# Performance work log

Measured on AMD Instinct MI355X. Metric: run time of the kernel, lower is better.

Reference implementation:

```python
import jax, jax.numpy as jnp
import numpy as np


def _leaky(x):
    return jnp.where(x >= 0, x, 0.01 * x)  # nn.LeakyReLU default slope


def _conv1x1(x, w):
    # x: [B, C, H, W], w: [O, C] (1x1 conv == per-pixel channel GEMM)
    return jnp.einsum('bchw,oc->bohw', x, w)


def setup_inputs() -> dict:
    key = jax.random.key(0)
    ks = jax.random.split(key, 12)

    def kaiming(k, o, c):  # kaiming_normal_ fan_out, relu gain, 1x1 kernel
        return jax.random.normal(k, (o, c), jnp.float32) * np.float32(np.sqrt(2.0 / o))

    lr_feature = jax.random.normal(ks[0], (1, 32, 256, 512), jnp.float32)
    hr_feature = jax.random.normal(ks[1], (1, 32, 512, 1024), jnp.float32)
    return {
        'lr_feature': lr_feature,
        'hr_feature': hr_feature,
        's1_w0': kaiming(ks[2], 128, 128),
        's1_w1': kaiming(ks[3], 64, 128),
        's1_w2': kaiming(ks[4], 32, 64),
        's1_w3': kaiming(ks[5], 16, 32),
        's1_w4': kaiming(ks[6], 8, 16),
        's1_w5': kaiming(ks[7], 1, 8),
        's2_w0': kaiming(ks[8], 3, 3),
        's2_w1': kaiming(ks[9], 2, 3),
        's2_w2': kaiming(ks[10], 1, 2),
        'fuse_w': jnp.ones((1, 2), jnp.float32),  # fuse weight initialized to 1
    }


def reference(lr_feature, hr_feature, s1_w0, s1_w1, s1_w2, s1_w3, s1_w4, s1_w5,
              s2_w0, s2_w1, s2_w2, fuse_w):
    scale = hr_feature.shape[-1] // lr_feature.shape[-1]  # static python int (=2, even)
    Hh, Wh = hr_feature.shape[-2], hr_feature.shape[-1]

    # nearest-neighbor upsample of lr_feature by `scale` (expand/view trick in torch)
    lr_up = jnp.repeat(jnp.repeat(lr_feature, scale, axis=2), scale, axis=3)

    # representation: [B, 128, Hh, Wh]
    rep = jnp.concatenate(
        [lr_up, hr_feature, lr_up * hr_feature, (lr_up - hr_feature) ** 2], axis=1)

    # similarity_measure1: 1x1-conv MLP chain 128->128->64->32->16->8->1
    o = _leaky(_conv1x1(rep, s1_w0))
    o = _leaky(_conv1x1(o, s1_w1))
    o = _leaky(_conv1x1(o, s1_w2))
    o = _leaky(_conv1x1(o, s1_w3))
    o = _conv1x1(o, s1_w4)
    weights1 = _conv1x1(o, s1_w5)  # [B, 1, Hh, Wh]

    # distance matrix (even-scale branch): 3 channels [dx, dy, norm]
    v = jnp.arange(-(scale // 2), scale // 2 + 1, dtype=jnp.float32)
    m = v.shape[0] // 2
    v = jnp.concatenate([v[:m], v[m + 1:]])  # drop center -> length `scale`
    d0 = jnp.broadcast_to(v[None, :], (scale, scale))
    dm = jnp.stack([d0, d0.T, jnp.sqrt(d0 ** 2 + d0.T ** 2)], axis=0)  # [3,s,s]
    dm = jnp.tile(dm, (1, Hh // scale, Wh // scale))[None]  # [1, 3, Hh, Wh]

    # similarity_measure2: 3->3->2->1
    w2 = _leaky(_conv1x1(dm, s2_w0))
    w2 = _leaky(_conv1x1(w2, s2_w1))
    weights2 = _conv1x1(w2, s2_w2)  # [1, 1, Hh, Wh]

    # fuse (weight forced non-negative via abs, as in forward's .data mutation)
    mapping = _conv1x1(jnp.concatenate([weights1, weights2], axis=1), jnp.abs(fuse_w))
    return mapping
```

## Files before the change

### kernel.cpp

```cpp
#include <hip/hip_runtime.h>

typedef short v8s __attribute__((ext_vector_type(8)));
typedef float v4f __attribute__((ext_vector_type(4)));

#define Wh   1024
#define HWh  (1024 * 512)
#define Wlr  512
#define HWlr (512 * 256)

#define THREADS 768
#define WAVES   12
#define NBLK    256
#define SLOTS   64
#define MAXIT   6

#define HALF_STRIDE 2052
#define ACT_SHORTS  (2 * HALF_STRIDE)
#define WF_N         53
#define WFRAG_SHORTS (WF_N * 512)
#define LDS_BYTES   ((WFRAG_SHORTS + WAVES * ACT_SHORTS) * 2)

__device__ __forceinline__ unsigned short f2bf(float f) {
    union { float f; unsigned u; } v; v.f = f;
    unsigned r = v.u + 0x7FFFu + ((v.u >> 16) & 1u);
    return (unsigned short)(r >> 16);
}
__device__ __forceinline__ unsigned pk2(float a, float b) {
    union { float f; unsigned u; } ua, ub;
    ua.f = a; ub.f = b;
    return __builtin_amdgcn_perm(ub.u + 0x8000u, ua.u + 0x8000u, 0x07060302u);
}
__device__ __forceinline__ float leaky(float x) { return fmaxf(x, 0.01f * x); }

__device__ __forceinline__ void ep_write(unsigned short* buf, int h, int c0, int p, uint2 v) {
    *(uint2*)(buf + h * HALF_STRIDE + (c0 >> 5) * 512 +
              (((c0 >> 3) & 3) * 16 + p) * 8 + (c0 & 7)) = v;
}
__device__ __forceinline__ void stq(unsigned short* buf, int px, int pass, int cq,
                                    int c, unsigned lo, unsigned hi) {
    *(uint2*)(buf + (px >> 4) * HALF_STRIDE + c * 512 +
              (pass * 16 + (px & 15)) * 8 + 4 * cq) = (uint2){lo, hi};
}

__global__ __launch_bounds__(THREADS, 3)
void cmfsm_kernel(const float* __restrict__ lr, const float* __restrict__ hr,
                  const float* __restrict__ w0g, const float* __restrict__ w1g,
                  const float* __restrict__ w2g, const float* __restrict__ w3g,
                  const float* __restrict__ w4g, const float* __restrict__ w5g,
                  const float* __restrict__ t0g, const float* __restrict__ t1g,
                  const float* __restrict__ t2g, const float* __restrict__ fwg,
                  float* __restrict__ out)
{
    extern __shared__ unsigned short smem[];
    unsigned short* wfrag = smem;
    unsigned short* actS  = smem + WFRAG_SHORTS;

    const int tid  = threadIdx.x;
    const int lane = tid & 63;
    const int wv   = tid >> 6;
    const int p    = lane & 15;
    const int q    = lane >> 4;
    const int px   = lane & 31;
    const int cq   = lane >> 5;

    for (int e = tid; e < 32 * 64; e += THREADS) {
        int f = e >> 6, l = e & 63;
        int mt = f >> 2, ks = f & 3, pp = l & 15, qq = l >> 4;
        const float* src = w0g + (mt * 16 + pp) * 128 + ks * 32 + qq * 8;
        unsigned short* dst = wfrag + f * 512 + l * 8;
#pragma unroll
        for (int j = 0; j < 8; ++j) dst[j] = f2bf(src[j]);
    }
    for (int e = tid; e < 16 * 64; e += THREADS) {
        int f = e >> 6, l = e & 63;
        int mt = f >> 2, ks = f & 3, pp = l & 15, qq = l >> 4;
        const float* src = w1g + (mt * 16 + pp) * 128 + ks * 32 + qq * 8;
        unsigned short* dst = wfrag + (32 + f) * 512 + l * 8;
#pragma unroll
        for (int j = 0; j < 8; ++j) dst[j] = f2bf(src[j]);
    }
    if (tid < 4 * 64) {
        int f = tid >> 6, l = tid & 63;
        int mt = f >> 1, ks = f & 1, pp = l & 15, qq = l >> 4;
        const float* src = w2g + (mt * 16 + pp) * 64 + ks * 32 + qq * 8;
        unsigned short* dst = wfrag + (48 + f) * 512 + l * 8;
#pragma unroll
        for (int j = 0; j < 8; ++j) dst[j] = f2bf(src[j]);
    }
    if (tid < 64) {
        int l = tid, pp = l & 15, qq = l >> 4;
        const float* src = w3g + pp * 32 + qq * 8;
        unsigned short* dst = wfrag + 52 * 512 + l * 8;
#pragma unroll
        for (int j = 0; j < 8; ++j) dst[j] = f2bf(src[j]);
    }

    float w45[4];
#pragma unroll
    for (int r = 0; r < 4; ++r) {
        float s = 0.f;
#pragma unroll
        for (int j = 0; j < 8; ++j) s += w5g[j] * w4g[j * 16 + q * 4 + r];
        w45[r] = s;
    }

    float w2tab[4];
#pragma unroll
    for (int yp = 0; yp < 2; ++yp)
#pragma unroll
        for (int xp = 0; xp < 2; ++xp) {
            float i0 = xp ? 1.f : -1.f;
            float i1 = yp ? 1.f : -1.f;
            float i2 = 1.41421356237309505f;
            float h0[3], h1[2];
            for (int o = 0; o < 3; ++o)
                h0[o] = leaky(t0g[o*3+0]*i0 + t0g[o*3+1]*i1 + t0g[o*3+2]*i2);
            for (int o = 0; o < 2; ++o)
                h1[o] = leaky(t1g[o*3+0]*h0[0] + t1g[o*3+1]*h0[1] + t1g[o*3+2]*h0[2]);
            w2tab[yp*2+xp] = t2g[0]*h1[0] + t2g[1]*h1[1];
        }
    const float fa = fabsf(fwg[0]);
    const float fb = fabsf(fwg[1]);

    __syncthreads();

    unsigned short* B = actS + wv * ACT_SHORTS;
    const v4f z4 = (v4f){0.f, 0.f, 0.f, 0.f};

    for (int it = 0; it < MAXIT; ++it) {
        const int s = it * WAVES + wv;
        if (s >= SLOTS) break;
        const int gbase = (blockIdx.x * SLOTS + s) * 32;
        const int y     = gbase >> 10;
        const float* hr_it = hr + gbase;
        const float* lr_it = lr + (y >> 1) * Wlr + ((gbase & 1023) >> 1);

#pragma unroll
        for (int pass = 0; pass < 4; ++pass) {
            const int ch = pass * 8 + cq * 4;
            float h0 = hr_it[(size_t)(ch + 0) * HWh + px];
            float h1 = hr_it[(size_t)(ch + 1) * HWh + px];
            float h2 = hr_it[(size_t)(ch + 2) * HWh + px];
            float h3 = hr_it[(size_t)(ch + 3) * HWh + px];
            float l0 = lr_it[(size_t)(ch + 0) * HWlr + (px >> 1)];
            float l1 = lr_it[(size_t)(ch + 1) * HWlr + (px >> 1)];
            float l2 = lr_it[(size_t)(ch + 2) * HWlr + (px >> 1)];
            float l3 = lr_it[(size_t)(ch + 3) * HWlr + (px >> 1)];
            stq(B, px, pass, cq, 0, pk2(l0, l1), pk2(l2, l3));
            stq(B, px, pass, cq, 1, pk2(h0, h1), pk2(h2, h3));
            stq(B, px, pass, cq, 2, pk2(l0*h0, l1*h1), pk2(l2*h2, l3*h3));
            float d0 = l0-h0, d1 = l1-h1, d2 = l2-h2, d3 = l3-h3;
            stq(B, px, pass, cq, 3, pk2(d0*d0, d1*d1), pk2(d2*d2, d3*d3));
        }

        {
            v8s bfr[4][2];
#pragma unroll
            for (int ks = 0; ks < 4; ++ks) {
                bfr[ks][0] = *(const v8s*)(B + ks * 512 + lane * 8);
                bfr[ks][1] = *(const v8s*)(B + HALF_STRIDE + ks * 512 + lane * 8);
            }
#pragma unroll
            for (int mh = 0; mh < 2; ++mh) {
                v4f acc[4][2];
#pragma unroll
                for (int ks = 0; ks < 4; ++ks)
#pragma unroll
                    for (int mi = 0; mi < 4; ++mi) {
                        v8s a = *(const v8s*)(wfrag + ((mh*4+mi)*4 + ks) * 512 + lane * 8);
                        acc[mi][0] = __builtin_amdgcn_mfma_f32_16x16x32_bf16(
                            a, bfr[ks][0], ks == 0 ? z4 : acc[mi][0], 0, 0, 0);
                        acc[mi][1] = __builtin_amdgcn_mfma_f32_16x16x32_bf16(
                            a, bfr[ks][1], ks == 0 ? z4 : acc[mi][1], 0, 0, 0);
                    }
#pragma unroll
                for (int mi = 0; mi < 4; ++mi) {
                    const int c0 = 16 * (mh * 4 + mi) + 4 * q;
#pragma unroll
                    for (int h = 0; h < 2; ++h) {
                        uint2 v;
                        v.x = pk2(leaky(acc[mi][h][0]), leaky(acc[mi][h][1]));
                        v.y = pk2(leaky(acc[mi][h][2]), leaky(acc[mi][h][3]));
                        ep_write(B, h, c0, p, v);
                    }
                }
            }
        }

        {
            v8s bfr[4][2];
#pragma unroll
            for (int ks = 0; ks < 4; ++ks) {
                bfr[ks][0] = *(const v8s*)(B + ks * 512 + lane * 8);
                bfr[ks][1] = *(const v8s*)(B + HALF_STRIDE + ks * 512 + lane * 8);
            }
            v4f acc[4][2];
#pragma unroll
            for (int ks = 0; ks < 4; ++ks)
#pragma unroll
                for (int mt = 0; mt < 4; ++mt) {
                    v8s a = *(const v8s*)(wfrag + (32 + mt*4 + ks) * 512 + lane * 8);
                    acc[mt][0] = __builtin_amdgcn_mfma_f32_16x16x32_bf16(
                        a, bfr[ks][0], ks == 0 ? z4 : acc[mt][0], 0, 0, 0);
                    acc[mt][1] = __builtin_amdgcn_mfma_f32_16x16x32_bf16(
                        a, bfr[ks][1], ks == 0 ? z4 : acc[mt][1], 0, 0, 0);
                }
#pragma unroll
            for (int mt = 0; mt < 4; ++mt) {
                const int c0 = 16 * mt + 4 * q;
#pragma unroll
                for (int h = 0; h < 2; ++h) {
                    uint2 v;
                    v.x = pk2(leaky(acc[mt][h][0]), leaky(acc[mt][h][1]));
                    v.y = pk2(leaky(acc[mt][h][2]), leaky(acc[mt][h][3]));
                    ep_write(B, h, c0, p, v);
                }
            }
        }

        {
            v8s bfr[2][2];
#pragma unroll
            for (int ks = 0; ks < 2; ++ks) {
                bfr[ks][0] = *(const v8s*)(B + ks * 512 + lane * 8);
                bfr[ks][1] = *(const v8s*)(B + HALF_STRIDE + ks * 512 + lane * 8);
            }
            v4f acc[2][2];
#pragma unroll
            for (int ks = 0; ks < 2; ++ks)
#pragma unroll
                for (int mt = 0; mt < 2; ++mt) {
                    v8s a = *(const v8s*)(wfrag + (48 + mt*2 + ks) * 512 + lane * 8);
                    acc[mt][0] = __builtin_amdgcn_mfma_f32_16x16x32_bf16(
                        a, bfr[ks][0], ks == 0 ? z4 : acc[mt][0], 0, 0, 0);
                    acc[mt][1] = __builtin_amdgcn_mfma_f32_16x16x32_bf16(
                        a, bfr[ks][1], ks == 0 ? z4 : acc[mt][1], 0, 0, 0);
                }
#pragma unroll
            for (int mt = 0; mt < 2; ++mt) {
                const int c0 = 16 * mt + 4 * q;
#pragma unroll
                for (int h = 0; h < 2; ++h) {
                    uint2 v;
                    v.x = pk2(leaky(acc[mt][h][0]), leaky(acc[mt][h][1]));
                    v.y = pk2(leaky(acc[mt][h][2]), leaky(acc[mt][h][3]));
                    ep_write(B, h, c0, p, v);
                }
            }
        }

        {
            v8s a = *(const v8s*)(wfrag + 52 * 512 + lane * 8);
            float res[2];
#pragma unroll
            for (int h = 0; h < 2; ++h) {
                v8s b = *(const v8s*)(B + h * HALF_STRIDE + lane * 8);
                v4f acc3 = __builtin_amdgcn_mfma_f32_16x16x32_bf16(a, b, z4, 0, 0, 0);
                float part = 0.f;
#pragma unroll
                for (int r = 0; r < 4; ++r) part += w45[r] * leaky(acc3[r]);
                part += __shfl_xor(part, 16, 64);
                part += __shfl_xor(part, 32, 64);
                res[h] = part;
            }
            const float wb = fb * w2tab[((y & 1) << 1) | (p & 1)];
            if (q == 0)      out[gbase + p]      = fa * res[0] + wb;
            else if (q == 1) out[gbase + 16 + p] = fa * res[1] + wb;
        }
    }
}

extern "C" void kernel_launch(void* const* d_in, const int* in_sizes, int n_in,
                              void* d_out, int out_size, void* d_ws, size_t ws_size,
                              hipStream_t stream) {
    const float* lr  = (const float*)d_in[0];
    const float* hr  = (const float*)d_in[1];
    const float* w0g = (const float*)d_in[2];
    const float* w1g = (const float*)d_in[3];
    const float* w2g = (const float*)d_in[4];
    const float* w3g = (const float*)d_in[5];
    const float* w4g = (const float*)d_in[6];
    const float* w5g = (const float*)d_in[7];
    const float* t0g = (const float*)d_in[8];
    const float* t1g = (const float*)d_in[9];
    const float* t2g = (const float*)d_in[10];
    const float* fwg = (const float*)d_in[11];
    float* out = (float*)d_out;

    hipLaunchKernelGGL(cmfsm_kernel, dim3(NBLK), dim3(THREADS), LDS_BYTES, stream,
                       lr, hr, w0g, w1g, w2g, w3g, w4g, w5g, t0g, t1g, t2g, fwg, out);
}
```

Baseline: 165.7 us.

## Move most weight fragments to global workspace and raise waves per block

A small prep kernel converts one fragment of w0 plus all of w1, w2 and w3 into bf16 MFMA fragment layout in the workspace. The main kernel then reads those fragments from global memory/cache instead of LDS, which shrinks the LDS weight area from 53 to 31 fragments. The freed LDS allows 16 waves per block, with exact even work division (4 iterations, no slot check) and the padded activation stride removed. The cost is an extra kernel launch, more global/L1 traffic per MFMA operand, and possible LDS bank conflicts now that the stride padding is gone.

```diff
diff --git a/kernel.cpp b/kernel.cpp
--- a/kernel.cpp
+++ b/kernel.cpp
@@ -8,17 +8,18 @@
 #define Wlr  512
 #define HWlr (512 * 256)
 
-#define THREADS 768
-#define WAVES   12
+#define THREADS 1024
+#define WAVES   16
 #define NBLK    256
-#define SLOTS   64
-#define MAXIT   6
-
-#define HALF_STRIDE 2052
+#define MAXIT   4
+
+#define HALF_STRIDE 2048
 #define ACT_SHORTS  (2 * HALF_STRIDE)
-#define WF_N         53
+#define WF_N         31
 #define WFRAG_SHORTS (WF_N * 512)
 #define LDS_BYTES   ((WFRAG_SHORTS + WAVES * ACT_SHORTS) * 2)
+
+#define WS_FRAGS 22
 
 __device__ __forceinline__ unsigned short f2bf(float f) {
     union { float f; unsigned u; } v; v.f = f;
@@ -42,13 +43,29 @@
               (pass * 16 + (px & 15)) * 8 + 4 * cq) = (uint2){lo, hi};
 }
 
-__global__ __launch_bounds__(THREADS, 3)
+__global__ void prep_kernel(const float* __restrict__ w0g, const float* __restrict__ w1g,
+                            const float* __restrict__ w2g, const float* __restrict__ w3g,
+                            unsigned short* __restrict__ ws)
+{
+    const int f = blockIdx.x;
+    const int l = threadIdx.x;
+    const int pp = l & 15, qq = l >> 4;
+    const float* src;
+    if (f == 0)       src = w0g + (7 * 16 + pp) * 128 + 3 * 32 + qq * 8;
+    else if (f < 17)  { int g = f - 1;  src = w1g + ((g >> 2) * 16 + pp) * 128 + (g & 3) * 32 + qq * 8; }
+    else if (f < 21)  { int g = f - 17; src = w2g + ((g >> 1) * 16 + pp) * 64  + (g & 1) * 32 + qq * 8; }
+    else              src = w3g + pp * 32 + qq * 8;
+    unsigned short* dst = ws + f * 512 + l * 8;
+#pragma unroll
+    for (int j = 0; j < 8; ++j) dst[j] = f2bf(src[j]);
+}
+
+__global__ __launch_bounds__(THREADS, 4)
 void cmfsm_kernel(const float* __restrict__ lr, const float* __restrict__ hr,
-                  const float* __restrict__ w0g, const float* __restrict__ w1g,
-                  const float* __restrict__ w2g, const float* __restrict__ w3g,
-                  const float* __restrict__ w4g, const float* __restrict__ w5g,
-                  const float* __restrict__ t0g, const float* __restrict__ t1g,
-                  const float* __restrict__ t2g, const float* __restrict__ fwg,
+                  const float* __restrict__ w0g, const float* __restrict__ w4g,
+                  const float* __restrict__ w5g, const float* __restrict__ t0g,
+                  const float* __restrict__ t1g, const float* __restrict__ t2g,
+                  const float* __restrict__ fwg, const unsigned short* __restrict__ wsf,
                   float* __restrict__ out)
 {
     extern __shared__ unsigned short smem[];
@@ -63,34 +80,11 @@
     const int px   = lane & 31;
     const int cq   = lane >> 5;
 
-    for (int e = tid; e < 32 * 64; e += THREADS) {
+    for (int e = tid; e < WF_N * 64; e += THREADS) {
         int f = e >> 6, l = e & 63;
         int mt = f >> 2, ks = f & 3, pp = l & 15, qq = l >> 4;
         const float* src = w0g + (mt * 16 + pp) * 128 + ks * 32 + qq * 8;
         unsigned short* dst = wfrag + f * 512 + l * 8;
-#pragma unroll
-        for (int j = 0; j < 8; ++j) dst[j] = f2bf(src[j]);
-    }
-    for (int e = tid; e < 16 * 64; e += THREADS) {
-        int f = e >> 6, l = e & 63;
-        int mt = f >> 2, ks = f & 3, pp = l & 15, qq = l >> 4;
-        const float* src = w1g + (mt * 16 + pp) * 128 + ks * 32 + qq * 8;
-        unsigned short* dst = wfrag + (32 + f) * 512 + l * 8;
-#pragma unroll
-        for (int j = 0; j < 8; ++j) dst[j] = f2bf(src[j]);
-    }
-    if (tid < 4 * 64) {
-        int f = tid >> 6, l = tid & 63;
-        int mt = f >> 1, ks = f & 1, pp = l & 15, qq = l >> 4;
-        const float* src = w2g + (mt * 16 + pp) * 64 + ks * 32 + qq * 8;
-        unsigned short* dst = wfrag + (48 + f) * 512 + l * 8;
-#pragma unroll
-        for (int j = 0; j < 8; ++j) dst[j] = f2bf(src[j]);
-    }
-    if (tid < 64) {
-        int l = tid, pp = l & 15, qq = l >> 4;
-        const float* src = w3g + pp * 32 + qq * 8;
-        unsigned short* dst = wfrag + 52 * 512 + l * 8;
 #pragma unroll
         for (int j = 0; j < 8; ++j) dst[j] = f2bf(src[j]);
     }
@@ -122,15 +116,16 @@
     const float fa = fabsf(fwg[0]);
     const float fb = fabsf(fwg[1]);
 
+    const unsigned short* wsl = wsf + lane * 8;
+
     __syncthreads();
 
     unsigned short* B = actS + wv * ACT_SHORTS;
     const v4f z4 = (v4f){0.f, 0.f, 0.f, 0.f};
 
+#pragma unroll 1
     for (int it = 0; it < MAXIT; ++it) {
-        const int s = it * WAVES + wv;
-        if (s >= SLOTS) break;
-        const int gbase = (blockIdx.x * SLOTS + s) * 32;
+        const int gbase = ((blockIdx.x * MAXIT + it) * WAVES + wv) * 32;
         const int y     = gbase >> 10;
         const float* hr_it = hr + gbase;
         const float* lr_it = lr + (y >> 1) * Wlr + ((gbase & 1023) >> 1);
@@ -160,6 +155,7 @@
                 bfr[ks][0] = *(const v8s*)(B + ks * 512 + lane * 8);
                 bfr[ks][1] = *(const v8s*)(B + HALF_STRIDE + ks * 512 + lane * 8);
             }
+            v8s w0f31 = *(const v8s*)(wsl + 0 * 512);
 #pragma unroll
             for (int mh = 0; mh < 2; ++mh) {
                 v4f acc[4][2];
@@ -167,7 +163,9 @@
                 for (int ks = 0; ks < 4; ++ks)
 #pragma unroll
                     for (int mi = 0; mi < 4; ++mi) {
-                        v8s a = *(const v8s*)(wfrag + ((mh*4+mi)*4 + ks) * 512 + lane * 8);
+                        const int f = (mh * 4 + mi) * 4 + ks;
+                        v8s a = (f == 31) ? w0f31
+                                          : *(const v8s*)(wfrag + f * 512 + lane * 8);
                         acc[mi][0] = __builtin_amdgcn_mfma_f32_16x16x32_bf16(
                             a, bfr[ks][0], ks == 0 ? z4 : acc[mi][0], 0, 0, 0);
                         acc[mi][1] = __builtin_amdgcn_mfma_f32_16x16x32_bf16(
@@ -196,15 +194,19 @@
             }
             v4f acc[4][2];
 #pragma unroll
-            for (int ks = 0; ks < 4; ++ks)
-#pragma unroll
-                for (int mt = 0; mt < 4; ++mt) {
-                    v8s a = *(const v8s*)(wfrag + (32 + mt*4 + ks) * 512 + lane * 8);
-                    acc[mt][0] = __builtin_amdgcn_mfma_f32_16x16x32_bf16(
-                        a, bfr[ks][0], ks == 0 ? z4 : acc[mt][0], 0, 0, 0);
-                    acc[mt][1] = __builtin_amdgcn_mfma_f32_16x16x32_bf16(
-                        a, bfr[ks][1], ks == 0 ? z4 : acc[mt][1], 0, 0, 0);
-                }
+            for (int ks = 0; ks < 4; ++ks) {
+                v8s a0 = *(const v8s*)(wsl + (1 + 0 * 4 + ks) * 512);
+                v8s a1 = *(const v8s*)(wsl + (1 + 1 * 4 + ks) * 512);
+                v8s a2 = *(const v8s*)(wsl + (1 + 2 * 4 + ks) * 512);
+                v8s a3 = *(const v8s*)(wsl + (1 + 3 * 4 + ks) * 512);
+#pragma unroll
+                for (int h = 0; h < 2; ++h) {
+                    acc[0][h] = __builtin_amdgcn_mfma_f32_16x16x32_bf16(a0, bfr[ks][h], ks == 0 ? z4 : acc[0][h], 0, 0, 0);
+                    acc[1][h] = __builtin_amdgcn_mfma_f32_16x16x32_bf16(a1, bfr[ks][h], ks == 0 ? z4 : acc[1][h], 0, 0, 0);
+                    acc[2][h] = __builtin_amdgcn_mfma_f32_16x16x32_bf16(a2, bfr[ks][h], ks == 0 ? z4 : acc[2][h], 0, 0, 0);
+                    acc[3][h] = __builtin_amdgcn_mfma_f32_16x16x32_bf16(a3, bfr[ks][h], ks == 0 ? z4 : acc[3][h], 0, 0, 0);
+                }
+            }
 #pragma unroll
             for (int mt = 0; mt < 4; ++mt) {
                 const int c0 = 16 * mt + 4 * q;
@@ -227,15 +229,15 @@
             }
             v4f acc[2][2];
 #pragma unroll
-            for (int ks = 0; ks < 2; ++ks)
-#pragma unroll
-                for (int mt = 0; mt < 2; ++mt) {
-                    v8s a = *(const v8s*)(wfrag + (48 + mt*2 + ks) * 512 + lane * 8);
-                    acc[mt][0] = __builtin_amdgcn_mfma_f32_16x16x32_bf16(
-                        a, bfr[ks][0], ks == 0 ? z4 : acc[mt][0], 0, 0, 0);
-                    acc[mt][1] = __builtin_amdgcn_mfma_f32_16x16x32_bf16(
-                        a, bfr[ks][1], ks == 0 ? z4 : acc[mt][1], 0, 0, 0);
-                }
+            for (int ks = 0; ks < 2; ++ks) {
+                v8s a0 = *(const v8s*)(wsl + (17 + 0 * 2 + ks) * 512);
+                v8s a1 = *(const v8s*)(wsl + (17 + 1 * 2 + ks) * 512);
+#pragma unroll
+                for (int h = 0; h < 2; ++h) {
+                    acc[0][h] = __builtin_amdgcn_mfma_f32_16x16x32_bf16(a0, bfr[ks][h], ks == 0 ? z4 : acc[0][h], 0, 0, 0);
+                    acc[1][h] = __builtin_amdgcn_mfma_f32_16x16x32_bf16(a1, bfr[ks][h], ks == 0 ? z4 : acc[1][h], 0, 0, 0);
+                }
+            }
 #pragma unroll
             for (int mt = 0; mt < 2; ++mt) {
                 const int c0 = 16 * mt + 4 * q;
@@ -250,7 +252,7 @@
         }
 
         {
-            v8s a = *(const v8s*)(wfrag + 52 * 512 + lane * 8);
+            v8s a = *(const v8s*)(wsl + 21 * 512);
             float res[2];
 #pragma unroll
             for (int h = 0; h < 2; ++h) {
@@ -286,7 +288,10 @@
     const float* t2g = (const float*)d_in[10];
     const float* fwg = (const float*)d_in[11];
     float* out = (float*)d_out;
-
+    unsigned short* wsf = (unsigned short*)d_ws;
+
+    hipLaunchKernelGGL(prep_kernel, dim3(WS_FRAGS), dim3(64), 0, stream,
+                       w0g, w1g, w2g, w3g, wsf);
     hipLaunchKernelGGL(cmfsm_kernel, dim3(NBLK), dim3(THREADS), LDS_BYTES, stream,
-                       lr, hr, w0g, w1g, w2g, w3g, w4g, w5g, t0g, t1g, t2g, fwg, out);
-}
+                       lr, hr, w0g, w4g, w5g, t0g, t1g, t2g, fwg, wsf, out);
+}
```

After: 277.6 us. +67.5%, slower.

## Build layer-0 MFMA operands in registers and prefetch next slot's inputs

Applied to the files above, without the earlier changes.

The input tile is now loaded directly in the MFMA B-operand lane layout, so the first layer's operands are packed in registers. This removes the LDS staging write and read-back for the 128-channel representation. The global loads for the next slot are issued before the MFMA chain of the current slot, overlapping memory latency with compute. In exchange, register pressure rises from 32 extra floats held across the loop, which could hurt occupancy at 3 blocks of 768 threads, and the last iteration redundantly reloads its own slot.

```diff
diff --git a/kernel.cpp b/kernel.cpp
--- a/kernel.cpp
+++ b/kernel.cpp
@@ -12,7 +12,6 @@
 #define WAVES   12
 #define NBLK    256
 #define SLOTS   64
-#define MAXIT   6
 
 #define HALF_STRIDE 2052
 #define ACT_SHORTS  (2 * HALF_STRIDE)
@@ -36,10 +35,24 @@
     *(uint2*)(buf + h * HALF_STRIDE + (c0 >> 5) * 512 +
               (((c0 >> 3) & 3) * 16 + p) * 8 + (c0 & 7)) = v;
 }
-__device__ __forceinline__ void stq(unsigned short* buf, int px, int pass, int cq,
-                                    int c, unsigned lo, unsigned hi) {
-    *(uint2*)(buf + (px >> 4) * HALF_STRIDE + c * 512 +
-              (pass * 16 + (px & 15)) * 8 + 4 * cq) = (uint2){lo, hi};
+
+__device__ __forceinline__ void ld32(const float* __restrict__ hr, const float* __restrict__ lr,
+                                     int gbase, int p, int q,
+                                     float (&h0)[8], float (&h1)[8],
+                                     float (&l0)[8], float (&l1)[8]) {
+    const int y  = gbase >> 10;
+    const int x0 = gbase & 1023;
+    const float* hb = hr + (size_t)y * Wh + x0 + p;
+    const float* lb = lr + (size_t)(y >> 1) * Wlr + (x0 >> 1) + (p >> 1);
+#pragma unroll
+    for (int j = 0; j < 8; ++j) {
+        const size_t hc = (size_t)(8 * q + j) * HWh;
+        const size_t lc = (size_t)(8 * q + j) * HWlr;
+        h0[j] = hb[hc];
+        h1[j] = hb[hc + 16];
+        l0[j] = lb[lc];
+        l1[j] = lb[lc + 8];
+    }
 }
 
 __global__ __launch_bounds__(THREADS, 3)
@@ -60,8 +73,6 @@
     const int wv   = tid >> 6;
     const int p    = lane & 15;
     const int q    = lane >> 4;
-    const int px   = lane & 31;
-    const int cq   = lane >> 5;
 
     for (int e = tid; e < 32 * 64; e += THREADS) {
         int f = e >> 6, l = e & 63;
@@ -127,83 +138,83 @@
     unsigned short* B = actS + wv * ACT_SHORTS;
     const v4f z4 = (v4f){0.f, 0.f, 0.f, 0.f};
 
-    for (int it = 0; it < MAXIT; ++it) {
-        const int s = it * WAVES + wv;
-        if (s >= SLOTS) break;
+    float xh0[8], xh1[8], xl0[8], xl1[8];
+    ld32(hr, lr, (blockIdx.x * SLOTS + wv) * 32, p, q, xh0, xh1, xl0, xl1);
+
+#pragma unroll 1
+    for (int s = wv; s < SLOTS; s += WAVES) {
         const int gbase = (blockIdx.x * SLOTS + s) * 32;
         const int y     = gbase >> 10;
-        const float* hr_it = hr + gbase;
-        const float* lr_it = lr + (y >> 1) * Wlr + ((gbase & 1023) >> 1);
-
-#pragma unroll
-        for (int pass = 0; pass < 4; ++pass) {
-            const int ch = pass * 8 + cq * 4;
-            float h0 = hr_it[(size_t)(ch + 0) * HWh + px];
-            float h1 = hr_it[(size_t)(ch + 1) * HWh + px];
-            float h2 = hr_it[(size_t)(ch + 2) * HWh + px];
-            float h3 = hr_it[(size_t)(ch + 3) * HWh + px];
-            float l0 = lr_it[(size_t)(ch + 0) * HWlr + (px >> 1)];
-            float l1 = lr_it[(size_t)(ch + 1) * HWlr + (px >> 1)];
-            float l2 = lr_it[(size_t)(ch + 2) * HWlr + (px >> 1)];
-            float l3 = lr_it[(size_t)(ch + 3) * HWlr + (px >> 1)];
-            stq(B, px, pass, cq, 0, pk2(l0, l1), pk2(l2, l3));
-            stq(B, px, pass, cq, 1, pk2(h0, h1), pk2(h2, h3));
-            stq(B, px, pass, cq, 2, pk2(l0*h0, l1*h1), pk2(l2*h2, l3*h3));
-            float d0 = l0-h0, d1 = l1-h1, d2 = l2-h2, d3 = l3-h3;
-            stq(B, px, pass, cq, 3, pk2(d0*d0, d1*d1), pk2(d2*d2, d3*d3));
+
+        v8s bfr[2][4];
+#pragma unroll
+        for (int hf = 0; hf < 2; ++hf) {
+            const float* hv = hf ? xh1 : xh0;
+            const float* lv = hf ? xl1 : xl0;
+            unsigned* b0 = (unsigned*)&bfr[hf][0];
+            unsigned* b1 = (unsigned*)&bfr[hf][1];
+            unsigned* b2 = (unsigned*)&bfr[hf][2];
+            unsigned* b3 = (unsigned*)&bfr[hf][3];
+#pragma unroll
+            for (int jj = 0; jj < 4; ++jj) {
+                float l0 = lv[2*jj], l1 = lv[2*jj+1];
+                float h0 = hv[2*jj], h1 = hv[2*jj+1];
+                b0[jj] = pk2(l0, l1);
+                b1[jj] = pk2(h0, h1);
+                b2[jj] = pk2(l0 * h0, l1 * h1);
+                float d0 = l0 - h0, d1 = l1 - h1;
+                b3[jj] = pk2(d0 * d0, d1 * d1);
+            }
         }
 
         {
-            v8s bfr[4][2];
+            const int ns = (s + WAVES < SLOTS) ? s + WAVES : s;
+            ld32(hr, lr, (blockIdx.x * SLOTS + ns) * 32, p, q, xh0, xh1, xl0, xl1);
+        }
+
+#pragma unroll
+        for (int mh = 0; mh < 2; ++mh) {
+            v4f acc[4][2];
+#pragma unroll
+            for (int ks = 0; ks < 4; ++ks)
+#pragma unroll
+                for (int mi = 0; mi < 4; ++mi) {
+                    v8s a = *(const v8s*)(wfrag + ((mh * 4 + mi) * 4 + ks) * 512 + lane * 8);
+                    acc[mi][0] = __builtin_amdgcn_mfma_f32_16x16x32_bf16(
+                        a, bfr[0][ks], ks == 0 ? z4 : acc[mi][0], 0, 0, 0);
+                    acc[mi][1] = __builtin_amdgcn_mfma_f32_16x16x32_bf16(
+                        a, bfr[1][ks], ks == 0 ? z4 : acc[mi][1], 0, 0, 0);
+                }
+#pragma unroll
+            for (int mi = 0; mi < 4; ++mi) {
+                const int c0 = 16 * (mh * 4 + mi) + 4 * q;
+#pragma unroll
+                for (int h = 0; h < 2; ++h) {
+                    uint2 v;
+                    v.x = pk2(leaky(acc[mi][h][0]), leaky(acc[mi][h][1]));
+                    v.y = pk2(leaky(acc[mi][h][2]), leaky(acc[mi][h][3]));
+                    ep_write(B, h, c0, p, v);
+                }
+            }
+        }
+
+        {
+            v8s bf[4][2];
 #pragma unroll
             for (int ks = 0; ks < 4; ++ks) {
-                bfr[ks][0] = *(const v8s*)(B + ks * 512 + lane * 8);
-                bfr[ks][1] = *(const v8s*)(B + HALF_STRIDE + ks * 512 + lane * 8);
-            }
-#pragma unroll
-            for (int mh = 0; mh < 2; ++mh) {
-                v4f acc[4][2];
-#pragma unroll
-                for (int ks = 0; ks < 4; ++ks)
-#pragma unroll
-                    for (int mi = 0; mi < 4; ++mi) {
-                        v8s a = *(const v8s*)(wfrag + ((mh*4+mi)*4 + ks) * 512 + lane * 8);
-                        acc[mi][0] = __builtin_amdgcn_mfma_f32_16x16x32_bf16(
-                            a, bfr[ks][0], ks == 0 ? z4 : acc[mi][0], 0, 0, 0);
-                        acc[mi][1] = __builtin_amdgcn_mfma_f32_16x16x32_bf16(
-                            a, bfr[ks][1], ks == 0 ? z4 : acc[mi][1], 0, 0, 0);
-                    }
-#pragma unroll
-                for (int mi = 0; mi < 4; ++mi) {
-                    const int c0 = 16 * (mh * 4 + mi) + 4 * q;
-#pragma unroll
-                    for (int h = 0; h < 2; ++h) {
-                        uint2 v;
-                        v.x = pk2(leaky(acc[mi][h][0]), leaky(acc[mi][h][1]));
-                        v.y = pk2(leaky(acc[mi][h][2]), leaky(acc[mi][h][3]));
-                        ep_write(B, h, c0, p, v);
-                    }
-                }
-            }
-        }
-
-        {
-            v8s bfr[4][2];
-#pragma unroll
-            for (int ks = 0; ks < 4; ++ks) {
-                bfr[ks][0] = *(const v8s*)(B + ks * 512 + lane * 8);
-                bfr[ks][1] = *(const v8s*)(B + HALF_STRIDE + ks * 512 + lane * 8);
+                bf[ks][0] = *(const v8s*)(B + ks * 512 + lane * 8);
+                bf[ks][1] = *(const v8s*)(B + HALF_STRIDE + ks * 512 + lane * 8);
             }
             v4f acc[4][2];
 #pragma unroll
             for (int ks = 0; ks < 4; ++ks)
 #pragma unroll
                 for (int mt = 0; mt < 4; ++mt) {
-                    v8s a = *(const v8s*)(wfrag + (32 + mt*4 + ks) * 512 + lane * 8);
+                    v8s a = *(const v8s*)(wfrag + (32 + mt * 4 + ks) * 512 + lane * 8);
                     acc[mt][0] = __builtin_amdgcn_mfma_f32_16x16x32_bf16(
-                        a, bfr[ks][0], ks == 0 ? z4 : acc[mt][0], 0, 0, 0);
+                        a, bf[ks][0], ks == 0 ? z4 : acc[mt][0], 0, 0, 0);
                     acc[mt][1] = __builtin_amdgcn_mfma_f32_16x16x32_bf16(
-                        a, bfr[ks][1], ks == 0 ? z4 : acc[mt][1], 0, 0, 0);
+                        a, bf[ks][1], ks == 0 ? z4 : acc[mt][1], 0, 0, 0);
                 }
 #pragma unroll
             for (int mt = 0; mt < 4; ++mt) {
@@ -219,22 +230,22 @@
         }
 
         {
-            v8s bfr[2][2];
+            v8s bf[2][2];
 #pragma unroll
             for (int ks = 0; ks < 2; ++ks) {
-                bfr[ks][0] = *(const v8s*)(B + ks * 512 + lane * 8);
-                bfr[ks][1] = *(const v8s*)(B + HALF_STRIDE + ks * 512 + lane * 8);
+                bf[ks][0] = *(const v8s*)(B + ks * 512 + lane * 8);
+                bf[ks][1] = *(const v8s*)(B + HALF_STRIDE + ks * 512 + lane * 8);
             }
             v4f acc[2][2];
 #pragma unroll
             for (int ks = 0; ks < 2; ++ks)
 #pragma unroll
                 for (int mt = 0; mt < 2; ++mt) {
-                    v8s a = *(const v8s*)(wfrag + (48 + mt*2 + ks) * 512 + lane * 8);
+                    v8s a = *(const v8s*)(wfrag + (48 + mt * 2 + ks) * 512 + lane * 8);
                     acc[mt][0] = __builtin_amdgcn_mfma_f32_16x16x32_bf16(
-                        a, bfr[ks][0], ks == 0 ? z4 : acc[mt][0], 0, 0, 0);
+                        a, bf[ks][0], ks == 0 ? z4 : acc[mt][0], 0, 0, 0);
                     acc[mt][1] = __builtin_amdgcn_mfma_f32_16x16x32_bf16(
-                        a, bfr[ks][1], ks == 0 ? z4 : acc[mt][1], 0, 0, 0);
+                        a, bf[ks][1], ks == 0 ? z4 : acc[mt][1], 0, 0, 0);
                 }
 #pragma unroll
             for (int mt = 0; mt < 2; ++mt) {
```

New measurement: 154.2 us. -7.0%, faster.
